# Performance work log

Hardware: AMD Instinct MI355X
Metric: run time of the kernel (lower is better)

## Reference

```python
import jax, jax.numpy as jnp
import numpy as np

BN_EPS = 1e-5

def _conv1x1(x, w, b=None):
    # x: [B,C,H,W], w: [O,C] -> [B,O,H,W]
    y = jnp.einsum('bchw,oc->bohw', x, w)
    if b is not None:
        y = y + b[None, :, None, None]
    return y

def _bn_silu(y, gamma, beta):
    # BN inference with running_mean=0, running_var=1, then SiLU
    scale = gamma / jnp.sqrt(1.0 + BN_EPS)
    y = y * scale[None, :, None, None] + beta[None, :, None, None]
    return jax.nn.silu(y)

def setup_inputs() -> dict:
    key = jax.random.key(0)
    ks = jax.random.split(key, 20)
    B, D, S = 32, 512, 32
    C = D // 2
    d = {}
    d['x'] = jax.random.normal(ks[0], (B, D, S, S), jnp.float32)
    d['cv1_w'] = jax.random.normal(ks[1], (C, D), jnp.float32) * (1.0 / np.sqrt(D))
    d['cv1_gamma'] = jax.random.uniform(ks[2], (C,), jnp.float32, 0.5, 1.5)
    d['cv1_beta'] = jax.random.normal(ks[3], (C,), jnp.float32) * 0.1
    d['q_w'] = jax.random.normal(ks[4], (C, C), jnp.float32) * (1.0 / np.sqrt(C))
    d['q_b'] = jax.random.normal(ks[5], (C,), jnp.float32) * 0.02
    d['k_w'] = jax.random.normal(ks[6], (C, C), jnp.float32) * (1.0 / np.sqrt(C))
    d['k_b'] = jax.random.normal(ks[7], (C,), jnp.float32) * 0.02
    d['v_w'] = jax.random.normal(ks[8], (C, C), jnp.float32) * (1.0 / np.sqrt(C))
    d['v_b'] = jax.random.normal(ks[9], (C,), jnp.float32) * 0.02
    d['e_w'] = jax.random.normal(ks[10], (C, C), jnp.float32) * (1.0 / np.sqrt(C))
    d['e_b'] = jax.random.normal(ks[11], (C,), jnp.float32) * 0.02
    d['rel_h'] = jax.random.normal(ks[12], (1, C, S, 1), jnp.float32)
    d['rel_w'] = jax.random.normal(ks[13], (1, C, 1, S), jnp.float32)
    d['cv2_w'] = jax.random.normal(ks[14], (D, C), jnp.float32) * (1.0 / np.sqrt(C))
    d['cv2_gamma'] = jax.random.uniform(ks[15], (D,), jnp.float32, 0.5, 1.5)
    d['cv2_beta'] = jax.random.normal(ks[16], (D,), jnp.float32) * 0.1
    return d

def reference(x, cv1_w, cv1_gamma, cv1_beta, q_w, q_b, k_w, k_b, v_w, v_b,
              e_w, e_b, rel_h, rel_w, cv2_w, cv2_gamma, cv2_beta):
    # cv1: 1x1 conv (no bias) + BN + SiLU
    x1 = _bn_silu(_conv1x1(x, cv1_w), cv1_gamma, cv1_beta)  # [B,C,H,W]
    B, C, H, W = x1.shape
    N = H * W
    q = _conv1x1(x1, q_w, q_b).reshape(B, C, N)
    k = _conv1x1(x1, k_w, k_b).reshape(B, C, N)
    v = _conv1x1(x1, v_w, v_b).reshape(B, C, N)
    e = _conv1x1(x1, e_w, e_b).reshape(B, C, N)
    # content-content: q^T k -> [B,N,N]
    cc = jnp.einsum('bci,bcj->bij', q, k)
    # content-position: (rel_h + rel_w) flattened to [C,N], times extra proj
    pos = (rel_h + rel_w).reshape(C, N)  # broadcast add -> [1,C,H,W] -> [C,N]
    cp = jnp.einsum('ci,bcj->bij', pos, e)  # [B,N,N]
    attn = jax.nn.softmax(cc + cp, axis=-1)
    # out[b,c,i] = sum_j v[b,c,j] * attn[b,i,j]
    out = jnp.einsum('bcj,bij->bci', v, attn).reshape(B, C, H, W)
    y = _bn_silu(_conv1x1(out, cv2_w), cv2_gamma, cv2_beta)
    return x + y
```

## Files before the change

kernel.cpp:

```cpp
#include <hip/hip_runtime.h>
#include <hip/hip_bf16.h>

typedef unsigned short u16;
typedef __attribute__((ext_vector_type(8))) _Float16 half8;
typedef __attribute__((ext_vector_type(4))) float f32x4;

__device__ __forceinline__ u16 f2h(float f) {
  _Float16 h = (_Float16)f;
  union { _Float16 h; u16 u; } a; a.h = h;
  return a.u;
}

__device__ __forceinline__ float h2f(u16 u) {
  union { _Float16 h; u16 u; } a; a.u = u;
  return (float)a.h;
}

__device__ __forceinline__ float silu_f(float y) {
  return y / (1.0f + __expf(-y));
}

__device__ __forceinline__ void glds16(const u16* g, u16* l) {
  __builtin_amdgcn_global_load_lds(
      (__attribute__((address_space(1))) unsigned*)(g),
      (__attribute__((address_space(3))) unsigned*)(l), 16, 0, 0);
}

enum { EPI_BNSILU_N = 0, EPI_QKEV, EPI_RAW_F16, EPI_BNSILU_RES_M };

template<int EPI, bool DUAL, int TILES, int GX>
__global__ __launch_bounds__(256, 3)
void gemm_nt(const u16* __restrict__ A, long long a_bs, int lda,
             const u16* __restrict__ A2,
             const u16* __restrict__ B, long long b_bs, int ldb,
             void* __restrict__ C0, long long c_bs, int ldc,
             void* __restrict__ C1, void* __restrict__ C2,
             int K,
             const float* __restrict__ p0, const float* __restrict__ p1,
             const float* __restrict__ res, long long res_bs)
{
  __shared__ u16 smem[8192];
  u16* lA = smem;
  u16* lB = smem + 4096;

  const int id = blockIdx.x;
  const int bz = (id & 7) + 8 * (id / (8 * TILES));
  const int tt = (id >> 3) % TILES;
  const int bm = tt % GX;
  const int bn = tt / GX;
  const u16* Ab = A + (long long)bz * a_bs;
  const u16* Bb = B + (long long)bz * b_bs;
  const int m0 = bm * 128;
  const int n0 = bn * 128;
  const int t = threadIdx.x;
  const int lane = t & 63;
  const int w = t >> 6;
  const int wm = (w & 1) * 64;
  const int wn = (w >> 1) * 64;
  const int q = lane >> 4;
  const int lr = lane & 15;

  f32x4 acc[4][4];
#pragma unroll
  for (int i = 0; i < 4; ++i)
#pragma unroll
    for (int j = 0; j < 4; ++j)
      acc[i][j] = (f32x4){0.f, 0.f, 0.f, 0.f};

  const int lrow = lane >> 2;
  const int kch = (lane & 3) ^ ((lane >> 2) & 3) ^ ((lane >> 4) & 3);
  const int lk = kch * 8;
  const u16* aR0 = Ab + (long long)(m0 + 32 * w + lrow) * lda + lk;
  const u16* aR1 = aR0 + 16LL * lda;
  const u16* bR0 = Bb + (long long)(n0 + 32 * w + lrow) * ldb + lk;
  const u16* bR1 = bR0 + 16LL * ldb;
  const u16* a2R0 = nullptr; const u16* a2R1 = nullptr;
  if constexpr (DUAL) {
    a2R0 = A2 + (long long)(m0 + 32 * w + lrow) * 256 + lk;
    a2R1 = a2R0 + 16LL * 256;
  }
  u16* la0 = lA + w * 1024; u16* la1 = la0 + 512;
  u16* lb0 = lB + w * 1024; u16* lb1 = lb0 + 512;
  const int fpos = (q ^ (lr & 3) ^ ((lr >> 2) & 3)) * 8;

  for (int k0 = 0; k0 < K; k0 += 32) {
    __syncthreads();
    if (!DUAL || k0 < 256) {
      glds16(aR0 + k0, la0);
      glds16(aR1 + k0, la1);
    } else {
      glds16(a2R0 + (k0 - 256), la0);
      glds16(a2R1 + (k0 - 256), la1);
    }
    glds16(bR0 + k0, lb0);
    glds16(bR1 + k0, lb1);
    __syncthreads();
    half8 af[4], bfr[4];
#pragma unroll
    for (int i = 0; i < 4; ++i)
      af[i] = *(const half8*)&lA[(wm + i * 16 + lr) * 32 + fpos];
#pragma unroll
    for (int j = 0; j < 4; ++j)
      bfr[j] = *(const half8*)&lB[(wn + j * 16 + lr) * 32 + fpos];
#pragma unroll
    for (int i = 0; i < 4; ++i)
#pragma unroll
      for (int j = 0; j < 4; ++j)
        acc[i][j] = __builtin_amdgcn_mfma_f32_16x16x32_f16(af[i], bfr[j], acc[i][j], 0, 0, 0);
  }

  if constexpr (EPI == EPI_BNSILU_N) {
    u16* Cg = (u16*)C0 + (long long)bz * c_bs;
#pragma unroll
    for (int i = 0; i < 4; ++i)
#pragma unroll
      for (int j = 0; j < 4; ++j)
#pragma unroll
        for (int r = 0; r < 4; ++r) {
          const int m = m0 + wm + i * 16 + q * 4 + r;
          const int n = n0 + wn + j * 16 + lr;
          float v = acc[i][j][r];
          v = silu_f(v * (p0[n] * 0.99999500003749969f) + p1[n]);
          Cg[(long long)m * ldc + n] = f2h(v);
        }
  } else if constexpr (EPI == EPI_RAW_F16) {
    u16* Cg = (u16*)C0 + (long long)bz * c_bs;
#pragma unroll
    for (int i = 0; i < 4; ++i)
#pragma unroll
      for (int j = 0; j < 4; ++j)
#pragma unroll
        for (int r = 0; r < 4; ++r) {
          const int m = m0 + wm + i * 16 + q * 4 + r;
          const int n = n0 + wn + j * 16 + lr;
          Cg[(long long)m * ldc + n] = f2h(acc[i][j][r]);
        }
  } else if constexpr (EPI == EPI_BNSILU_RES_M) {
    float* Cg = (float*)C0 + (long long)bz * c_bs;
    const float* rg = res + (long long)bz * res_bs;
#pragma unroll
    for (int i = 0; i < 4; ++i)
#pragma unroll
      for (int j = 0; j < 4; ++j)
#pragma unroll
        for (int r = 0; r < 4; ++r) {
          const int m = m0 + wm + i * 16 + q * 4 + r;
          const int n = n0 + wn + j * 16 + lr;
          float v = acc[i][j][r];
          v = silu_f(v * (p0[m] * 0.99999500003749969f) + p1[m]);
          const long long idx = (long long)m * ldc + n;
          Cg[idx] = v + rg[idx];
        }
  } else {
    const int seg = n0 >> 8;
    const int nb = n0 & 255;
    if (seg < 3) {
      u16* dst; long long bs; int ld2;
      if (seg == 0) { dst = (u16*)C0; bs = 262144; ld2 = 256; }
      else { dst = (u16*)C1 + (seg == 2 ? 256 : 0); bs = 524288; ld2 = 512; }
      dst += (long long)bz * bs;
#pragma unroll
      for (int i = 0; i < 4; ++i)
#pragma unroll
        for (int j = 0; j < 4; ++j)
#pragma unroll
          for (int r = 0; r < 4; ++r) {
            const int m = m0 + wm + i * 16 + q * 4 + r;
            const int col = wn + j * 16 + lr;
            float v = acc[i][j][r] + p0[n0 + col];
            dst[(long long)m * ld2 + nb + col] = f2h(v);
          }
    } else {
      u16* dst = (u16*)C2 + (long long)bz * 262144;
#pragma unroll
      for (int s = 0; s < 4; ++s) {
        const int rbase = s * 32;
        __syncthreads();
        if (wm == (rbase & 64)) {
          const int ibase = (rbase & 32) >> 4;
#pragma unroll
          for (int ii = 0; ii < 2; ++ii) {
            const int i = ibase + ii;
#pragma unroll
            for (int j = 0; j < 4; ++j)
#pragma unroll
              for (int r = 0; r < 4; ++r) {
                const int row32 = i * 16 + q * 4 + r - (rbase & 32);
                const int col = wn + j * 16 + lr;
                float v = acc[i][j][r] + p0[768 + nb + col];
                smem[row32 * 132 + col] = f2h(v);
              }
          }
        }
        __syncthreads();
#pragma unroll
        for (int p = 0; p < 2; ++p) {
          const int lin = p * 256 + t;
          const int c = lin >> 2;
          const int mc = lin & 3;
          u16 tmp[8];
#pragma unroll
          for (int r8 = 0; r8 < 8; ++r8)
            tmp[r8] = smem[(mc * 8 + r8) * 132 + c];
          *(half8*)&dst[(long long)(nb + c) * 1024 + m0 + rbase + mc * 8] =
              *(const half8*)tmp;
        }
      }
    }
  }
}

__global__ __launch_bounds__(256)
void transpose_x(const float* __restrict__ x, u16* __restrict__ xT) {
  __shared__ float tile[64][33];
  const int b = blockIdx.z;
  const int n0 = blockIdx.x * 32;
  const int d0 = blockIdx.y * 64;
  const int tx = threadIdx.x;
  const int ty = threadIdx.y;
  const float* src = x + (long long)b * 524288;
#pragma unroll
  for (int i = 0; i < 8; ++i)
    tile[ty + 8 * i][tx] = src[(long long)(d0 + ty + 8 * i) * 1024 + n0 + tx];
  __syncthreads();
  u16* dst = xT + (long long)b * 524288;
#pragma unroll
  for (int i = 0; i < 4; ++i) {
    const int n = ty + 8 * i;
    unsigned lo = (unsigned)f2h(tile[2 * tx][n]);
    unsigned hi = (unsigned)f2h(tile[2 * tx + 1][n]);
    *(unsigned*)&dst[(long long)(n0 + n) * 512 + d0 + 2 * tx] = lo | (hi << 16);
  }
}

__global__ __launch_bounds__(256)
void convert_w(const float* __restrict__ w1, const float* __restrict__ wq,
               const float* __restrict__ wk, const float* __restrict__ wv,
               const float* __restrict__ we, const float* __restrict__ w2,
               const float* __restrict__ bq, const float* __restrict__ bk,
               const float* __restrict__ be, const float* __restrict__ bv,
               u16* __restrict__ dstw, float* __restrict__ bbuf) {
  int id = blockIdx.x * 256 + threadIdx.x;
  if (id < 524288) {
    float v;
    if (id < 131072) v = w1[id];
    else if (id < 393216) {
      int s = id - 131072, o = s >> 8, c = s & 255;
      if (o < 256) v = wq[o * 256 + c];
      else if (o < 512) v = wk[(o - 256) * 256 + c];
      else if (o < 768) v = we[(o - 512) * 256 + c];
      else v = wv[(o - 768) * 256 + c];
    } else v = w2[id - 393216];
    dstw[id] = f2h(v);
  } else {
    int i = id - 524288;
    float v;
    if (i < 256) v = bq[i];
    else if (i < 512) v = bk[i - 256];
    else if (i < 768) v = be[i - 512];
    else v = bv[i - 768];
    bbuf[i] = v;
  }
}

__global__ __launch_bounds__(256)
void pos_compute(const float* __restrict__ rh, const float* __restrict__ rw,
                 u16* __restrict__ posT) {
  const int n = blockIdx.x;
  const int c = threadIdx.x;
  posT[n * 256 + c] = f2h(rh[c * 32 + (n >> 5)] + rw[c * 32 + (n & 31)]);
}

__global__ __launch_bounds__(256)
void softmax_rows(u16* __restrict__ logits) {
  __shared__ float red[8];
  u16* p = logits + (long long)blockIdx.x * 1024;
  const int t = threadIdx.x;
  ushort4 raw = ((const ushort4*)p)[t];
  float v0 = h2f(raw.x), v1 = h2f(raw.y), v2 = h2f(raw.z), v3 = h2f(raw.w);
  float mx = fmaxf(fmaxf(v0, v1), fmaxf(v2, v3));
#pragma unroll
  for (int off = 32; off > 0; off >>= 1) mx = fmaxf(mx, __shfl_down(mx, off));
  const int lane = t & 63, w = t >> 6;
  if (lane == 0) red[w] = mx;
  __syncthreads();
  mx = fmaxf(fmaxf(red[0], red[1]), fmaxf(red[2], red[3]));
  float e0 = __expf(v0 - mx), e1 = __expf(v1 - mx),
        e2 = __expf(v2 - mx), e3 = __expf(v3 - mx);
  float s = e0 + e1 + e2 + e3;
#pragma unroll
  for (int off = 32; off > 0; off >>= 1) s += __shfl_down(s, off);
  if (lane == 0) red[4 + w] = s;
  __syncthreads();
  const float inv = 1.0f / (red[4] + red[5] + red[6] + red[7]);
  ushort4 o;
  o.x = f2h(e0 * inv); o.y = f2h(e1 * inv); o.z = f2h(e2 * inv); o.w = f2h(e3 * inv);
  ((ushort4*)p)[t] = o;
}

extern "C" void kernel_launch(void* const* d_in, const int* in_sizes, int n_in,
                              void* d_out, int out_size, void* d_ws, size_t ws_size,
                              hipStream_t stream) {
  const float* x  = (const float*)d_in[0];
  const float* w1 = (const float*)d_in[1];
  const float* g1 = (const float*)d_in[2];
  const float* b1 = (const float*)d_in[3];
  const float* wq = (const float*)d_in[4];
  const float* bq = (const float*)d_in[5];
  const float* wk = (const float*)d_in[6];
  const float* bk = (const float*)d_in[7];
  const float* wv = (const float*)d_in[8];
  const float* bv = (const float*)d_in[9];
  const float* we = (const float*)d_in[10];
  const float* be = (const float*)d_in[11];
  const float* rh = (const float*)d_in[12];
  const float* rw = (const float*)d_in[13];
  const float* w2 = (const float*)d_in[14];
  const float* g2 = (const float*)d_in[15];
  const float* b2 = (const float*)d_in[16];
  float* out = (float*)d_out;
  char* ws = (char*)d_ws;

  u16* xT     = (u16*)(ws + 0);
  u16* x1t    = (u16*)(ws + 33554432);
  u16* qbuf   = (u16*)(ws + 50331648);
  u16* kcat   = (u16*)(ws + 67108864);
  u16* vbuf   = (u16*)(ws + 100663296);
  u16* outt   = (u16*)(ws + 117440512);
  u16* posT   = (u16*)(ws + 134217728);
  u16* wbuf   = (u16*)(ws + 134742016);
  float* bbuf = (float*)(ws + 135790592);
  u16* logits = (u16*)(ws + 142606336);

  u16* w1b    = wbuf;
  u16* wqkve  = wbuf + 131072;
  u16* w2b    = wbuf + 393216;

  transpose_x<<<dim3(32, 8, 32), dim3(32, 8), 0, stream>>>(x, xT);
  convert_w<<<dim3(2052), 256, 0, stream>>>(w1, wq, wk, wv, we, w2,
                                            bq, bk, be, bv, wbuf, bbuf);
  pos_compute<<<dim3(1024), 256, 0, stream>>>(rh, rw, posT);

  gemm_nt<EPI_BNSILU_N, false, 16, 8><<<dim3(512), 256, 0, stream>>>(
      xT, 524288LL, 512, nullptr, w1b, 0LL, 512,
      x1t, 262144LL, 256, nullptr, nullptr, 512, g1, b1, nullptr, 0LL);

  gemm_nt<EPI_QKEV, false, 64, 8><<<dim3(2048), 256, 0, stream>>>(
      x1t, 262144LL, 256, nullptr, wqkve, 0LL, 256,
      qbuf, 262144LL, 256, kcat, vbuf, 256, bbuf, nullptr, nullptr, 0LL);

  gemm_nt<EPI_RAW_F16, true, 64, 8><<<dim3(2048), 256, 0, stream>>>(
      qbuf, 262144LL, 256, posT, kcat, 524288LL, 512,
      logits, 1048576LL, 1024, nullptr, nullptr, 512, nullptr, nullptr, nullptr, 0LL);

  softmax_rows<<<dim3(32768), 256, 0, stream>>>(logits);

  gemm_nt<EPI_RAW_F16, false, 16, 8><<<dim3(512), 256, 0, stream>>>(
      logits, 1048576LL, 1024, nullptr, vbuf, 262144LL, 1024,
      outt, 262144LL, 256, nullptr, nullptr, 1024, nullptr, nullptr, nullptr, 0LL);

  gemm_nt<EPI_BNSILU_RES_M, false, 32, 4><<<dim3(1024), 256, 0, stream>>>(
      w2b, 0LL, 256, nullptr, outt, 262144LL, 256,
      out, 524288LL, 1024, nullptr, nullptr, 256, g2, b2, x, 524288LL);
}
```

Before: 332.5 us.

## Double-buffer LDS tiles in GEMM main loop with explicit waitcnt and barriers

Replaces the single-buffered load-sync-compute loop with a two-stage LDS ping-pong. The next K-slice is issued via global_load_lds while MFMAs run on the current buffer, with manual vmcnt/lgkmcnt waits and raw s_barrier in place of __syncthreads. It also raises wave priority around the MFMA block. This doubles LDS use to 32KB per block, which may lower occupancy, and assumes K is a multiple of 64.

```diff
diff --git a/kernel.cpp b/kernel.cpp
--- a/kernel.cpp
+++ b/kernel.cpp
@@ -39,9 +39,7 @@
              const float* __restrict__ p0, const float* __restrict__ p1,
              const float* __restrict__ res, long long res_bs)
 {
-  __shared__ u16 smem[8192];
-  u16* lA = smem;
-  u16* lB = smem + 4096;
+  __shared__ u16 smem[16384];
 
   const int id = blockIdx.x;
   const int bz = (id & 7) + 8 * (id / (8 * TILES));
@@ -79,35 +77,64 @@
     a2R0 = A2 + (long long)(m0 + 32 * w + lrow) * 256 + lk;
     a2R1 = a2R0 + 16LL * 256;
   }
-  u16* la0 = lA + w * 1024; u16* la1 = la0 + 512;
-  u16* lb0 = lB + w * 1024; u16* lb1 = lb0 + 512;
+  u16* const buf0 = smem;
+  u16* const buf1 = smem + 8192;
+  const int woff = w << 10;
   const int fpos = (q ^ (lr & 3) ^ ((lr >> 2) & 3)) * 8;
 
-  for (int k0 = 0; k0 < K; k0 += 32) {
-    __syncthreads();
-    if (!DUAL || k0 < 256) {
-      glds16(aR0 + k0, la0);
-      glds16(aR1 + k0, la1);
+#define STAGE(kk, base)                                                      \
+  do {                                                                       \
+    u16* _la = (base) + woff;                                                \
+    u16* _lb = (base) + 4096 + woff;                                         \
+    if (!DUAL || (kk) < 256) {                                               \
+      glds16(aR0 + (kk), _la);                                               \
+      glds16(aR1 + (kk), _la + 512);                                         \
+    } else {                                                                 \
+      glds16(a2R0 + ((kk) - 256), _la);                                      \
+      glds16(a2R1 + ((kk) - 256), _la + 512);                                \
+    }                                                                        \
+    glds16(bR0 + (kk), _lb);                                                 \
+    glds16(bR1 + (kk), _lb + 512);                                           \
+  } while (0)
+
+#define COMPUTE(base)                                                        \
+  do {                                                                       \
+    half8 af[4], bfr[4];                                                     \
+    _Pragma("unroll")                                                        \
+    for (int i = 0; i < 4; ++i)                                              \
+      af[i] = *(const half8*)&(base)[(wm + i * 16 + lr) * 32 + fpos];        \
+    _Pragma("unroll")                                                        \
+    for (int j = 0; j < 4; ++j)                                              \
+      bfr[j] = *(const half8*)&(base)[4096 + (wn + j * 16 + lr) * 32 + fpos];\
+    asm volatile("s_waitcnt lgkmcnt(0)" ::: "memory");                       \
+    __builtin_amdgcn_s_barrier();                                            \
+    __builtin_amdgcn_s_setprio(1);                                           \
+    _Pragma("unroll")                                                        \
+    for (int i = 0; i < 4; ++i)                                              \
+      _Pragma("unroll")                                                      \
+      for (int j = 0; j < 4; ++j)                                            \
+        acc[i][j] = __builtin_amdgcn_mfma_f32_16x16x32_f16(af[i], bfr[j],    \
+                                                           acc[i][j], 0,0,0);\
+    __builtin_amdgcn_s_setprio(0);                                           \
+  } while (0)
+
+  STAGE(0, buf0);
+  for (int k0 = 0; k0 < K; k0 += 64) {
+    STAGE(k0 + 32, buf1);
+    asm volatile("s_waitcnt vmcnt(4)" ::: "memory");
+    __builtin_amdgcn_s_barrier();
+    COMPUTE(buf0);
+    if (k0 + 64 < K) {
+      STAGE(k0 + 64, buf0);
+      asm volatile("s_waitcnt vmcnt(4)" ::: "memory");
     } else {
-      glds16(a2R0 + (k0 - 256), la0);
-      glds16(a2R1 + (k0 - 256), la1);
+      asm volatile("s_waitcnt vmcnt(0)" ::: "memory");
     }
-    glds16(bR0 + k0, lb0);
-    glds16(bR1 + k0, lb1);
-    __syncthreads();
-    half8 af[4], bfr[4];
-#pragma unroll
-    for (int i = 0; i < 4; ++i)
-      af[i] = *(const half8*)&lA[(wm + i * 16 + lr) * 32 + fpos];
-#pragma unroll
-    for (int j = 0; j < 4; ++j)
-      bfr[j] = *(const half8*)&lB[(wn + j * 16 + lr) * 32 + fpos];
-#pragma unroll
-    for (int i = 0; i < 4; ++i)
-#pragma unroll
-      for (int j = 0; j < 4; ++j)
-        acc[i][j] = __builtin_amdgcn_mfma_f32_16x16x32_f16(af[i], bfr[j], acc[i][j], 0, 0, 0);
-  }
+    __builtin_amdgcn_s_barrier();
+    COMPUTE(buf1);
+  }
+#undef STAGE
+#undef COMPUTE
 
   if constexpr (EPI == EPI_BNSILU_N) {
     u16* Cg = (u16*)C0 + (long long)bz * c_bs;
```

Result: slower. 347.7 us (+4.6%).
